# Performance work log

Measured on AMD Instinct MI355X. Metric: run time of the kernel, lower is better.

Reference implementation:

```python
import jax, jax.numpy as jnp
import numpy as np

SQRT_N = 32
SQRT_D = 32
B, N, D = 32, SQRT_N ** 2, SQRT_D ** 2  # batch, seq, d_model
LN_EPS = 1e-5


def _perm(x, s):
    # rearrange '... (m n) -> ... (n m)' with n = s
    shp = x.shape
    return x.reshape(*shp[:-1], -1, s).swapaxes(-1, -2).reshape(shp)


def _blockdiag_matmul(x, w):
    # w: [blocks, n, m]; x viewed as [..., blocks, m]
    s = w.shape[0]
    xv = x.reshape(*x.shape[:-1], s, w.shape[-1])
    return jnp.einsum('bnm,...bm->...bn', w, xv).reshape(x.shape)


def _monarch(x, L, R, s):
    x = _perm(x, s)
    x = _blockdiag_matmul(x, L)
    x = _perm(x, s)
    x = _blockdiag_matmul(x, R)
    return _perm(x, s)


def setup_inputs() -> dict:
    key = jax.random.key(0)
    ks = jax.random.split(key, 12)
    p = lambda k, s: (jax.random.normal(ks[k], (s, s, s), dtype=jnp.float32) * (1.0 / np.sqrt(s)))
    return {
        'x': jax.random.normal(ks[0], (B, N, D), dtype=jnp.float32),
        'm1_L': p(1, SQRT_N), 'm1_R': p(2, SQRT_N),
        'm2_L': p(3, SQRT_N), 'm2_R': p(4, SQRT_N),
        'm3_L': p(5, SQRT_D), 'm3_R': p(6, SQRT_D),
        'm4_L': p(7, SQRT_D), 'm4_R': p(8, SQRT_D),
        'n_kernel': jax.random.normal(ks[9], (SQRT_D ** 2, SQRT_N ** 2), dtype=jnp.float32),
        'd_kernel': jax.random.normal(ks[10], (1, SQRT_D ** 2), dtype=jnp.float32),
        'ln_gamma': jnp.ones((SQRT_D ** 2,), dtype=jnp.float32),
        'ln_beta': jnp.zeros((SQRT_D ** 2,), dtype=jnp.float32),
    }


def reference(x, m1_L, m1_R, m2_L, m2_R, m3_L, m3_R, m4_L, m4_R,
              n_kernel, d_kernel, ln_gamma, ln_beta):
    b, n, d = x.shape
    n2, d2 = SQRT_N ** 2, SQRT_D ** 2
    # pad sequence dim to sqrt_n^2
    x = jnp.pad(x, ((0, 0), (0, n2 - n), (0, 0)))
    # sequence (n) mixing, operating on [b, d, n2]
    xt = x.swapaxes(-1, -2)
    xt = _monarch(xt, m1_L, m1_R, SQRT_N)
    xt = jax.nn.relu(n_kernel * xt)
    xt = _monarch(xt, m2_L, m2_R, SQRT_N)
    x_tilde = xt.swapaxes(-1, -2)[:, :n, :]
    # pad feature dim to sqrt_d^2
    x_tilde = jnp.pad(x_tilde, ((0, 0), (0, 0), (0, d2 - x_tilde.shape[-1])))
    # feature (d) mixing
    y = _monarch(x_tilde, m3_L, m3_R, SQRT_D)
    y = jax.nn.relu(d_kernel * y)
    y = _monarch(y, m4_L, m4_R, SQRT_D)
    y = y[..., :d]
    # residual + LayerNorm over last dim (biased variance, eps=1e-5)
    h = y + x_tilde
    mu = jnp.mean(h, axis=-1, keepdims=True)
    var = jnp.mean(jnp.square(h - mu), axis=-1, keepdims=True)
    return (h - mu) * jax.lax.rsqrt(var + LN_EPS) * ln_gamma + ln_beta
```

## Files before the change

### kernel.cpp

```cpp
#include <hip/hip_runtime.h>


struct EpiNone {
  __device__ __forceinline__ void operator()(float2&, int, int) const {}
};
struct EpiReluNK {
  const float* nkp;
  __device__ __forceinline__ void operator()(float2& v, int n, int l2) const {
    float a = v.x * nkp[((size_t)l2 << 10) + n];
    float b = v.y * nkp[((size_t)(l2 + 1) << 10) + n];
    v.x = a > 0.f ? a : 0.f;
    v.y = b > 0.f ? b : 0.f;
  }
};
struct EpiReluDK {
  const float* dk;
  __device__ __forceinline__ void operator()(float2& v, int n, int) const {
    float w = dk[n];
    float a = v.x * w, b = v.y * w;
    v.x = a > 0.f ? a : 0.f;
    v.y = b > 0.f ? b : 0.f;
  }
};
struct EpiResid {
  const float* xtp;
  __device__ __forceinline__ void operator()(float2& v, int n, int l2) const {
    v.x += xtp[((size_t)l2 << 10) + n];
    v.y += xtp[((size_t)(l2 + 1) << 10) + n];
  }
};

template <class Epi>
__device__ __forceinline__ void monarch16(float* tile,
                                          const float* __restrict__ L,
                                          const float* __restrict__ R,
                                          int tid, const Epi& epi) {
  {
    const int g2 = (tid & 7) << 1;
    const int p = (tid >> 3) & 31;
    const int r0 = (tid >> 8) << 4;
    const int CA = (p << 4) + (g2 ^ (((p >> 2) & 7) << 1));
    float2 X[32];
#pragma unroll
    for (int j = 0; j < 32; ++j)
      X[j] = *(const float2*)&tile[(j << 9) + CA];
    __syncthreads();
    const float* Wp = L + (p << 10) + (r0 << 5);
#pragma unroll
    for (int i = 0; i < 16; ++i) {
      const float4* w4 = (const float4*)(Wp + (i << 5));
      float ax = 0.f, ay = 0.f;
#pragma unroll
      for (int q = 0; q < 8; ++q) {
        float4 w = w4[q];
        ax = fmaf(w.x, X[4 * q + 0].x, ax); ay = fmaf(w.x, X[4 * q + 0].y, ay);
        ax = fmaf(w.y, X[4 * q + 1].x, ax); ay = fmaf(w.y, X[4 * q + 1].y, ay);
        ax = fmaf(w.z, X[4 * q + 2].x, ax); ay = fmaf(w.z, X[4 * q + 2].y, ay);
        ax = fmaf(w.w, X[4 * q + 3].x, ax); ay = fmaf(w.w, X[4 * q + 3].y, ay);
      }
      float2 o; o.x = ax; o.y = ay;
      *(float2*)&tile[((r0 + i) << 9) + CA] = o;
    }
  }
  __syncthreads();
  {
    const int g2 = (tid & 7) << 1;
    const int r = (tid >> 3) & 31;
    const int u0 = (tid >> 8) << 4;
    float2 M[32];
    {
      const int rbase = r << 9;
#pragma unroll
      for (int p = 0; p < 32; ++p)
        M[p] = *(const float2*)&tile[rbase + (p << 4) + (g2 ^ (((p >> 2) & 7) << 1))];
    }
    __syncthreads();
    const float* Wr = R + (r << 10) + (u0 << 5);
    const int CB = (r << 4) + (g2 ^ (((r >> 2) & 7) << 1));
#pragma unroll
    for (int i = 0; i < 16; ++i) {
      const float4* w4 = (const float4*)(Wr + (i << 5));
      float ax = 0.f, ay = 0.f;
#pragma unroll
      for (int q = 0; q < 8; ++q) {
        float4 w = w4[q];
        ax = fmaf(w.x, M[4 * q + 0].x, ax); ay = fmaf(w.x, M[4 * q + 0].y, ay);
        ax = fmaf(w.y, M[4 * q + 1].x, ax); ay = fmaf(w.y, M[4 * q + 1].y, ay);
        ax = fmaf(w.z, M[4 * q + 2].x, ax); ay = fmaf(w.z, M[4 * q + 2].y, ay);
        ax = fmaf(w.w, M[4 * q + 3].x, ax); ay = fmaf(w.w, M[4 * q + 3].y, ay);
      }
      float2 o; o.x = ax; o.y = ay;
      const int n = ((u0 + i) << 5) + r;
      epi(o, n, g2);
      *(float2*)&tile[((u0 + i) << 9) + CB] = o;
    }
  }
  __syncthreads();
}

__global__ __launch_bounds__(512, 4) void p1_kernel(
    const float* __restrict__ x, const float* __restrict__ m1L,
    const float* __restrict__ m1R, const float* __restrict__ m2L,
    const float* __restrict__ m2R, const float* __restrict__ nk,
    float* __restrict__ xt_out) {
  extern __shared__ float tile[];
  const int b = blockIdx.y, d0 = blockIdx.x << 4;
  const int tid = (int)threadIdx.x;
  const float* xb = x + ((size_t)b << 20);
  {
    const int gq = tid & 3, qq = tid >> 2;
    const int A = (gq << 2) ^ (((qq >> 2) & 7) << 1);
#pragma unroll
    for (int j = 0; j < 8; ++j) {
      const int n = (j << 7) + qq;
      float4 v = *(const float4*)&xb[((size_t)n << 10) + d0 + (gq << 2)];
      float2 lo; lo.x = v.x; lo.y = v.y;
      float2 hi; hi.x = v.z; hi.y = v.w;
      *(float2*)&tile[(n << 4) + A] = lo;
      *(float2*)&tile[(n << 4) + (A ^ 2)] = hi;
    }
  }
  __syncthreads();
  EpiReluNK e1; e1.nkp = nk + ((size_t)d0 << 10);
  monarch16(tile, m1L, m1R, tid, e1);
  EpiNone e0;
  monarch16(tile, m2L, m2R, tid, e0);
  {
    const int gq = tid & 3, qq = tid >> 2;
    const int A = (gq << 2) ^ (((qq >> 2) & 7) << 1);
    float* ob = xt_out + ((size_t)b << 20);
#pragma unroll
    for (int j = 0; j < 8; ++j) {
      const int n = (j << 7) + qq;
      float2 lo = *(const float2*)&tile[(n << 4) + A];
      float2 hi = *(const float2*)&tile[(n << 4) + (A ^ 2)];
      float4 v; v.x = lo.x; v.y = lo.y; v.z = hi.x; v.w = hi.y;
      *(float4*)&ob[((size_t)n << 10) + d0 + (gq << 2)] = v;
    }
  }
}

__global__ __launch_bounds__(512, 4) void p2_kernel(
    const float* xt, const float* __restrict__ m3L,
    const float* __restrict__ m3R, const float* __restrict__ m4L,
    const float* __restrict__ m4R, const float* __restrict__ dk,
    const float* __restrict__ gamma, const float* __restrict__ beta,
    float* out) {
  extern __shared__ float tile[];
  const int b = blockIdx.y, n0 = blockIdx.x << 4;
  const int tid = (int)threadIdx.x;
  const float* xtp = xt + ((((size_t)b << 10) + n0) << 10);
  {
    const int l = tid & 15, qq = tid >> 4;
    const float* xr = xtp + ((size_t)l << 10);
    const int C3 = l ^ ((qq & 7) << 1);
#pragma unroll
    for (int j = 0; j < 8; ++j) {
      const int d = (j << 7) + (qq << 2);
      float4 v = *(const float4*)&xr[d];
      tile[((d + 0) << 4) + C3] = v.x;
      tile[((d + 1) << 4) + C3] = v.y;
      tile[((d + 2) << 4) + C3] = v.z;
      tile[((d + 3) << 4) + C3] = v.w;
    }
  }
  __syncthreads();
  EpiReluDK e3; e3.dk = dk;
  monarch16(tile, m3L, m3R, tid, e3);
  EpiResid e4; e4.xtp = xtp;
  monarch16(tile, m4L, m4R, tid, e4);
  {
    const int q = tid & 31, l = tid >> 5;
    const int base = (q << 4) + (l ^ (((q >> 2) & 7) << 1));
    float vbuf[32];
    float s = 0.f;
#pragma unroll
    for (int j = 0; j < 32; ++j) {
      vbuf[j] = tile[(j << 9) + base];
      s += vbuf[j];
    }
#pragma unroll
    for (int m = 1; m <= 16; m <<= 1) s += __shfl_xor(s, m);
    const float mu = s * (1.f / 1024.f);
    float vs = 0.f;
#pragma unroll
    for (int j = 0; j < 32; ++j) {
      float d = vbuf[j] - mu;
      vs += d * d;
    }
#pragma unroll
    for (int m = 1; m <= 16; m <<= 1) vs += __shfl_xor(vs, m);
    const float rs = rsqrtf(vs * (1.f / 1024.f) + 1e-5f);
    float* orow = out + ((((size_t)b << 10) + n0 + l) << 10);
#pragma unroll
    for (int j = 0; j < 32; ++j) {
      const int n = (j << 5) + q;
      orow[n] = (vbuf[j] - mu) * rs * gamma[n] + beta[n];
    }
  }
}

extern "C" void kernel_launch(void* const* d_in, const int* in_sizes, int n_in,
                              void* d_out, int out_size, void* d_ws, size_t ws_size,
                              hipStream_t stream) {
  (void)in_sizes; (void)n_in; (void)out_size; (void)d_ws; (void)ws_size;
  const float* x   = (const float*)d_in[0];
  const float* m1L = (const float*)d_in[1];
  const float* m1R = (const float*)d_in[2];
  const float* m2L = (const float*)d_in[3];
  const float* m2R = (const float*)d_in[4];
  const float* m3L = (const float*)d_in[5];
  const float* m3R = (const float*)d_in[6];
  const float* m4L = (const float*)d_in[7];
  const float* m4R = (const float*)d_in[8];
  const float* nk  = (const float*)d_in[9];
  const float* dk  = (const float*)d_in[10];
  const float* gam = (const float*)d_in[11];
  const float* bet = (const float*)d_in[12];
  float* out = (float*)d_out;

  dim3 grid(64, 32), block(512);
  const size_t lds = 1024 * 16 * sizeof(float);
  hipLaunchKernelGGL(p1_kernel, grid, block, lds, stream,
                     x, m1L, m1R, m2L, m2R, nk, out);
  hipLaunchKernelGGL(p2_kernel, grid, block, lds, stream,
                     out, m3L, m3R, m4L, m4R, dk, gam, bet, out);
}
```

Baseline: 1.087 ms.

## Widen Monarch tiles to 32 columns with 1024-thread blocks and new swizzle

Each block now processes 32 columns (feature or sequence rows) instead of 16, using 1024 threads and a 128 KB static LDS tile with a new XOR swizzle. Global accesses become 128-byte contiguous segments per row rather than 64-byte ones. The n_kernel ReLU scaling is moved into a separate LDS pass, and the residual add is folded into the LayerNorm load. The cost is larger LDS use per block, which limits residency to one block per CU and halves the grid size. Static shared allocation above 64 KB may also depend on the target allowing it.

Measured after the change: 922.6 us. -15.2%, faster.

```diff
diff --git a/kernel.cpp b/kernel.cpp
--- a/kernel.cpp
+++ b/kernel.cpp
@@ -1,54 +1,42 @@
 #include <hip/hip_runtime.h>
 
 
+#define TILE_ELEMS (1024 * 32)
+
 struct EpiNone {
-  __device__ __forceinline__ void operator()(float2&, int, int) const {}
-};
-struct EpiReluNK {
-  const float* nkp;
-  __device__ __forceinline__ void operator()(float2& v, int n, int l2) const {
-    float a = v.x * nkp[((size_t)l2 << 10) + n];
-    float b = v.y * nkp[((size_t)(l2 + 1) << 10) + n];
-    v.x = a > 0.f ? a : 0.f;
-    v.y = b > 0.f ? b : 0.f;
-  }
+  __device__ __forceinline__ void operator()(float2&, int) const {}
 };
 struct EpiReluDK {
   const float* dk;
-  __device__ __forceinline__ void operator()(float2& v, int n, int) const {
+  __device__ __forceinline__ void operator()(float2& v, int n) const {
     float w = dk[n];
     float a = v.x * w, b = v.y * w;
     v.x = a > 0.f ? a : 0.f;
     v.y = b > 0.f ? b : 0.f;
   }
 };
-struct EpiResid {
-  const float* xtp;
-  __device__ __forceinline__ void operator()(float2& v, int n, int l2) const {
-    v.x += xtp[((size_t)l2 << 10) + n];
-    v.y += xtp[((size_t)(l2 + 1) << 10) + n];
-  }
-};
 
 template <class Epi>
-__device__ __forceinline__ void monarch16(float* tile,
+__device__ __forceinline__ void monarch32(float* tile,
                                           const float* __restrict__ L,
                                           const float* __restrict__ R,
-                                          int tid, const Epi& epi) {
-  {
-    const int g2 = (tid & 7) << 1;
-    const int p = (tid >> 3) & 31;
-    const int r0 = (tid >> 8) << 4;
-    const int CA = (p << 4) + (g2 ^ (((p >> 2) & 7) << 1));
+                                          int tid, const Epi epi) {
+  const int l2 = (tid & 15) << 1;
+  const int pr = (tid >> 4) & 31;
+  const int h  = tid >> 9;
+  const int pb = pr << 5;
+  const int blA = l2 ^ (((pr >> 2) & 7) << 2);
+  const int blB = l2 ^ ((pr & 7) << 2);
+  {
     float2 X[32];
 #pragma unroll
     for (int j = 0; j < 32; ++j)
-      X[j] = *(const float2*)&tile[(j << 9) + CA];
+      X[j] = *(const float2*)&tile[(j << 10) + pb + (blA ^ ((j & 7) << 2))];
     __syncthreads();
-    const float* Wp = L + (p << 10) + (r0 << 5);
+    const float* Lp = L + (pr << 10) + (h << 9);
 #pragma unroll
     for (int i = 0; i < 16; ++i) {
-      const float4* w4 = (const float4*)(Wp + (i << 5));
+      const float4* w4 = (const float4*)(Lp + (i << 5));
       float ax = 0.f, ay = 0.f;
 #pragma unroll
       for (int q = 0; q < 8; ++q) {
@@ -58,28 +46,22 @@
         ax = fmaf(w.z, X[4 * q + 2].x, ax); ay = fmaf(w.z, X[4 * q + 2].y, ay);
         ax = fmaf(w.w, X[4 * q + 3].x, ax); ay = fmaf(w.w, X[4 * q + 3].y, ay);
       }
+      const int c = (h << 4) + i;
       float2 o; o.x = ax; o.y = ay;
-      *(float2*)&tile[((r0 + i) << 9) + CA] = o;
-    }
-  }
-  __syncthreads();
-  {
-    const int g2 = (tid & 7) << 1;
-    const int r = (tid >> 3) & 31;
-    const int u0 = (tid >> 8) << 4;
+      *(float2*)&tile[(c << 10) + pb + (blA ^ ((c & 7) << 2))] = o;
+    }
+  }
+  __syncthreads();
+  {
     float2 M[32];
-    {
-      const int rbase = r << 9;
-#pragma unroll
-      for (int p = 0; p < 32; ++p)
-        M[p] = *(const float2*)&tile[rbase + (p << 4) + (g2 ^ (((p >> 2) & 7) << 1))];
-    }
+#pragma unroll
+    for (int m = 0; m < 32; ++m)
+      M[m] = *(const float2*)&tile[(pr << 10) + (m << 5) + (blB ^ ((m >> 2) << 2))];
     __syncthreads();
-    const float* Wr = R + (r << 10) + (u0 << 5);
-    const int CB = (r << 4) + (g2 ^ (((r >> 2) & 7) << 1));
+    const float* Rp = R + (pr << 10) + (h << 9);
 #pragma unroll
     for (int i = 0; i < 16; ++i) {
-      const float4* w4 = (const float4*)(Wr + (i << 5));
+      const float4* w4 = (const float4*)(Rp + (i << 5));
       float ax = 0.f, ay = 0.f;
 #pragma unroll
       for (int q = 0; q < 8; ++q) {
@@ -89,95 +71,104 @@
         ax = fmaf(w.z, M[4 * q + 2].x, ax); ay = fmaf(w.z, M[4 * q + 2].y, ay);
         ax = fmaf(w.w, M[4 * q + 3].x, ax); ay = fmaf(w.w, M[4 * q + 3].y, ay);
       }
+      const int u = (h << 4) + i;
+      const int n = (u << 5) + pr;
       float2 o; o.x = ax; o.y = ay;
-      const int n = ((u0 + i) << 5) + r;
-      epi(o, n, g2);
-      *(float2*)&tile[((u0 + i) << 9) + CB] = o;
-    }
-  }
-  __syncthreads();
-}
-
-__global__ __launch_bounds__(512, 4) void p1_kernel(
+      epi(o, n);
+      *(float2*)&tile[(u << 10) + pb + (blA ^ ((u & 7) << 2))] = o;
+    }
+  }
+  __syncthreads();
+}
+
+__global__ __launch_bounds__(1024, 4) void p1_kernel(
     const float* __restrict__ x, const float* __restrict__ m1L,
     const float* __restrict__ m1R, const float* __restrict__ m2L,
     const float* __restrict__ m2R, const float* __restrict__ nk,
     float* __restrict__ xt_out) {
-  extern __shared__ float tile[];
-  const int b = blockIdx.y, d0 = blockIdx.x << 4;
+  __shared__ float tile[TILE_ELEMS];
+  const int b = blockIdx.y, d0 = blockIdx.x << 5;
   const int tid = (int)threadIdx.x;
-  const float* xb = x + ((size_t)b << 20);
-  {
-    const int gq = tid & 3, qq = tid >> 2;
-    const int A = (gq << 2) ^ (((qq >> 2) & 7) << 1);
+  {
+    const int g4 = tid & 7, nn = tid >> 3, l4 = g4 << 2;
+    const float* xb = x + ((size_t)b << 20) + d0 + l4;
 #pragma unroll
     for (int j = 0; j < 8; ++j) {
-      const int n = (j << 7) + qq;
-      float4 v = *(const float4*)&xb[((size_t)n << 10) + d0 + (gq << 2)];
-      float2 lo; lo.x = v.x; lo.y = v.y;
-      float2 hi; hi.x = v.z; hi.y = v.w;
-      *(float2*)&tile[(n << 4) + A] = lo;
-      *(float2*)&tile[(n << 4) + (A ^ 2)] = hi;
-    }
-  }
-  __syncthreads();
-  EpiReluNK e1; e1.nkp = nk + ((size_t)d0 << 10);
-  monarch16(tile, m1L, m1R, tid, e1);
-  EpiNone e0;
-  monarch16(tile, m2L, m2R, tid, e0);
-  {
-    const int gq = tid & 3, qq = tid >> 2;
-    const int A = (gq << 2) ^ (((qq >> 2) & 7) << 1);
-    float* ob = xt_out + ((size_t)b << 20);
+      const int n = (j << 7) + nn;
+      float4 v = *(const float4*)&xb[(size_t)n << 10];
+      const int t = ((n >> 2) ^ (n >> 5)) & 7;
+      *(float4*)&tile[(n << 5) + (l4 ^ (t << 2))] = v;
+    }
+  }
+  __syncthreads();
+  monarch32(tile, m1L, m1R, tid, EpiNone());
+  {
+    const int q = tid & 31, l = tid >> 5;
+    const int bl = l ^ (((q >> 2) & 7) << 2);
+    const float* nkr = nk + ((size_t)(d0 + l) << 10);
+#pragma unroll
+    for (int j = 0; j < 32; ++j) {
+      const int n = (j << 5) + q;
+      const int a = (j << 10) + (q << 5) + (bl ^ ((j & 7) << 2));
+      float v = tile[a] * nkr[n];
+      tile[a] = v > 0.f ? v : 0.f;
+    }
+  }
+  __syncthreads();
+  monarch32(tile, m2L, m2R, tid, EpiNone());
+  {
+    const int g4 = tid & 7, nn = tid >> 3, l4 = g4 << 2;
+    float* ob = xt_out + ((size_t)b << 20) + d0 + l4;
 #pragma unroll
     for (int j = 0; j < 8; ++j) {
-      const int n = (j << 7) + qq;
-      float2 lo = *(const float2*)&tile[(n << 4) + A];
-      float2 hi = *(const float2*)&tile[(n << 4) + (A ^ 2)];
-      float4 v; v.x = lo.x; v.y = lo.y; v.z = hi.x; v.w = hi.y;
-      *(float4*)&ob[((size_t)n << 10) + d0 + (gq << 2)] = v;
-    }
-  }
-}
-
-__global__ __launch_bounds__(512, 4) void p2_kernel(
+      const int n = (j << 7) + nn;
+      const int t = ((n >> 2) ^ (n >> 5)) & 7;
+      float4 v = *(const float4*)&tile[(n << 5) + (l4 ^ (t << 2))];
+      *(float4*)&ob[(size_t)n << 10] = v;
+    }
+  }
+}
+
+__global__ __launch_bounds__(1024, 4) void p2_kernel(
     const float* xt, const float* __restrict__ m3L,
     const float* __restrict__ m3R, const float* __restrict__ m4L,
     const float* __restrict__ m4R, const float* __restrict__ dk,
     const float* __restrict__ gamma, const float* __restrict__ beta,
     float* out) {
-  extern __shared__ float tile[];
-  const int b = blockIdx.y, n0 = blockIdx.x << 4;
+  __shared__ float tile[TILE_ELEMS];
+  const int b = blockIdx.y, n0 = blockIdx.x << 5;
   const int tid = (int)threadIdx.x;
-  const float* xtp = xt + ((((size_t)b << 10) + n0) << 10);
-  {
-    const int l = tid & 15, qq = tid >> 4;
-    const float* xr = xtp + ((size_t)l << 10);
-    const int C3 = l ^ ((qq & 7) << 1);
-#pragma unroll
-    for (int j = 0; j < 8; ++j) {
-      const int d = (j << 7) + (qq << 2);
-      float4 v = *(const float4*)&xr[d];
-      tile[((d + 0) << 4) + C3] = v.x;
-      tile[((d + 1) << 4) + C3] = v.y;
-      tile[((d + 2) << 4) + C3] = v.z;
-      tile[((d + 3) << 4) + C3] = v.w;
+  const float* xrows = xt + ((((size_t)b << 10) + n0) << 10);
+  {
+    const int c = tid & 255, lg = tid >> 8;
+    const int t = (c ^ (c >> 3)) & 7;
+#pragma unroll
+    for (int k = 0; k < 8; ++k) {
+      const int l = (lg << 3) + k;
+      float4 v = *(const float4*)&xrows[((size_t)l << 10) + (c << 2)];
+      const int lx = l ^ (t << 2);
+      tile[(c << 7) + lx] = v.x;
+      tile[(c << 7) + 32 + lx] = v.y;
+      tile[(c << 7) + 64 + lx] = v.z;
+      tile[(c << 7) + 96 + lx] = v.w;
     }
   }
   __syncthreads();
   EpiReluDK e3; e3.dk = dk;
-  monarch16(tile, m3L, m3R, tid, e3);
-  EpiResid e4; e4.xtp = xtp;
-  monarch16(tile, m4L, m4R, tid, e4);
+  monarch32(tile, m3L, m3R, tid, e3);
+  monarch32(tile, m4L, m4R, tid, EpiNone());
   {
     const int q = tid & 31, l = tid >> 5;
-    const int base = (q << 4) + (l ^ (((q >> 2) & 7) << 1));
-    float vbuf[32];
+    const int bl = l ^ (((q >> 2) & 7) << 2);
+    const float* xr = xrows + ((size_t)l << 10);
+    float hbuf[32];
     float s = 0.f;
 #pragma unroll
     for (int j = 0; j < 32; ++j) {
-      vbuf[j] = tile[(j << 9) + base];
-      s += vbuf[j];
+      const int n = (j << 5) + q;
+      float hv = tile[(j << 10) + (q << 5) + (bl ^ ((j & 7) << 2))] + xr[n];
+      hbuf[j] = hv;
+      s += hv;
     }
 #pragma unroll
     for (int m = 1; m <= 16; m <<= 1) s += __shfl_xor(s, m);
@@ -185,8 +176,8 @@
     float vs = 0.f;
 #pragma unroll
     for (int j = 0; j < 32; ++j) {
-      float d = vbuf[j] - mu;
-      vs += d * d;
+      float d = hbuf[j] - mu;
+      vs = fmaf(d, d, vs);
     }
 #pragma unroll
     for (int m = 1; m <= 16; m <<= 1) vs += __shfl_xor(vs, m);
@@ -195,7 +186,7 @@
 #pragma unroll
     for (int j = 0; j < 32; ++j) {
       const int n = (j << 5) + q;
-      orow[n] = (vbuf[j] - mu) * rs * gamma[n] + beta[n];
+      orow[n] = (hbuf[j] - mu) * rs * gamma[n] + beta[n];
     }
   }
 }
@@ -219,10 +210,9 @@
   const float* bet = (const float*)d_in[12];
   float* out = (float*)d_out;
 
-  dim3 grid(64, 32), block(512);
-  const size_t lds = 1024 * 16 * sizeof(float);
-  hipLaunchKernelGGL(p1_kernel, grid, block, lds, stream,
+  dim3 grid(32, 32), block(1024);
+  hipLaunchKernelGGL(p1_kernel, grid, block, 0, stream,
                      x, m1L, m1R, m2L, m2R, nk, out);
-  hipLaunchKernelGGL(p2_kernel, grid, block, lds, stream,
+  hipLaunchKernelGGL(p2_kernel, grid, block, 0, stream,
                      out, m3L, m3R, m4L, m4R, dk, gam, bet, out);
 }
```
